# Optimization experiments

Measured on AMD Instinct MI355X. Metric: run time of the kernel, lower is better.

Reference implementation:

```python
import jax, jax.numpy as jnp
import numpy as np

WINDOW_SIZE = 7
L = 255.0
C1 = (0.01 * L) ** 2
C2 = (0.03 * L) ** 2


def _box_filter(x, window):
    # x: [B,1,H,W], window: [1,1,k,k] (uniform 1/k^2). VALID conv, groups=1.
    return jax.lax.conv_general_dilated(
        x, window, window_strides=(1, 1), padding='VALID',
        dimension_numbers=('NCHW', 'OIHW', 'NCHW'))


def setup_inputs() -> dict:
    key = jax.random.key(0)
    k1, k2 = jax.random.split(key)
    shape = (16, 1, 1080, 1920)
    img1 = jax.random.uniform(k1, shape, dtype=jnp.float32) * L
    img2 = jax.random.uniform(k2, shape, dtype=jnp.float32) * L
    window = jnp.ones((1, 1, WINDOW_SIZE, WINDOW_SIZE), dtype=jnp.float32) / (WINDOW_SIZE * WINDOW_SIZE)
    return {"img1": img1, "img2": img2, "window": window}


def reference(img1, img2, window):
    mu1 = _box_filter(img1, window)
    mu2 = _box_filter(img2, window)
    mu1_sq = mu1 * mu1
    mu2_sq = mu2 * mu2
    mu1_mu2 = mu1 * mu2
    sigma1_sq = _box_filter(img1 * img1, window) - mu1_sq
    sigma2_sq = _box_filter(img2 * img2, window) - mu2_sq
    sigma12 = _box_filter(img1 * img2, window) - mu1_mu2
    v1 = 2.0 * sigma12 + C2
    v2 = sigma1_sq + sigma2_sq + C2
    ssim_map = (2.0 * mu1_mu2 + C1) * v1 / ((mu1_sq + mu2_sq + C1) * v2)
    return jnp.mean(ssim_map)
```

## Files before the change

kernel.cpp:

```cpp
#include <hip/hip_runtime.h>


constexpr int W_IN = 1920, H_IN = 1080;
constexpr int WOUT = W_IN - 6;
constexpr int HOUT = H_IN - 6;
constexpr int NBATCH = 16;
constexpr int WCOLS = 244;
constexpr int TW = 4 * WCOLS;
constexpr int TH = 71;
constexpr int NBX = 2, NBY = 16;
constexpr int NBLK = NBX * NBY * NBATCH;

constexpr float C1f = 6.5025f;
constexpr float C2f = 58.5225f;
constexpr float INV49 = 1.0f / 49.0f;

__device__ __forceinline__ float bperm(int addr, float v) {
  return __int_as_float(__builtin_amdgcn_ds_bpermute(addr, __float_as_int(v)));
}

__global__ __attribute__((amdgpu_flat_work_group_size(256, 256),
                          amdgpu_waves_per_eu(2, 2)))
void ssim_kernel(const float* __restrict__ img1, const float* __restrict__ img2,
                 double* __restrict__ partial) {
  const int t = threadIdx.x;
  const int lane = t & 63;
  const int xw = blockIdx.x * TW + (t >> 6) * WCOLS;
  const int y0 = blockIdx.y * TH;
  const size_t ib = (size_t)blockIdx.z * (size_t)(H_IN * W_IN);
  const float* __restrict__ p1 = img1 + ib;
  const float* __restrict__ p2 = img2 + ib;

  const int gcol = min(xw + 4 * lane, W_IN - 4);
  const int up1 = ((lane + 1) & 63) << 2;
  const int up2 = ((lane + 2) & 63) << 2;
  const bool lv = lane < 61;
  const bool m0 = lv && (xw + 4 * lane + 0 < WOUT);
  const bool m1 = lv && (xw + 4 * lane + 1 < WOUT);
  const bool m2 = lv && (xw + 4 * lane + 2 < WOUT);
  const bool m3 = lv && (xw + 4 * lane + 3 < WOUT);

#define DECLR(Q, C)                                                          \
  float R##Q##_##C##_0 = 0.f, R##Q##_##C##_1 = 0.f, R##Q##_##C##_2 = 0.f,    \
        R##Q##_##C##_3 = 0.f, R##Q##_##C##_4 = 0.f, R##Q##_##C##_5 = 0.f,    \
        R##Q##_##C##_6 = 0.f;
  DECLR(1, 0) DECLR(1, 1) DECLR(1, 2) DECLR(1, 3)
  DECLR(2, 0) DECLR(2, 1) DECLR(2, 2) DECLR(2, 3)
  DECLR(3, 0) DECLR(3, 1) DECLR(3, 2) DECLR(3, 3)
  DECLR(4, 0) DECLR(4, 1) DECLR(4, 2) DECLR(4, 3)
  DECLR(5, 0) DECLR(5, 1) DECLR(5, 2) DECLR(5, 3)
#undef DECLR
#define DECLV(Q) float V##Q##_0 = 0.f, V##Q##_1 = 0.f, V##Q##_2 = 0.f, V##Q##_3 = 0.f;
  DECLV(1) DECLV(2) DECLV(3) DECLV(4) DECLV(5)
#undef DECLV

  float accv = 0.f;

  float4 Aa = *(const float4*)(p1 + (size_t)y0 * W_IN + gcol);
  float4 Ab = *(const float4*)(p2 + (size_t)y0 * W_IN + gcol);
  float4 Ba, Bb;
  int gyn = y0 + 1;
  int oy = y0;

#define QC(Q, C, J)                                                         \
  { V##Q##_##C += s - R##Q##_##C##_##J; R##Q##_##C##_##J = s; }

#define EPI1(VA, VB, VAA, VBB, VAB, MASK)                                   \
  {                                                                         \
    const float mu1 = (VA) * INV49, mu2 = (VB) * INV49;                     \
    const float mu1s = mu1 * mu1, mu2s = mu2 * mu2, mu12 = mu1 * mu2;       \
    const float sg1 = fmaf((VAA), INV49, -mu1s);                            \
    const float sg2 = fmaf((VBB), INV49, -mu2s);                            \
    const float sg12 = fmaf((VAB), INV49, -mu12);                           \
    const float v1 = fmaf(2.f, sg12, C2f);                                  \
    const float v2 = sg1 + sg2 + C2f;                                       \
    const float num = fmaf(2.f, mu12, C1f) * v1;                            \
    const float den = (mu1s + mu2s + C1f) * v2;                             \
    const float ss = num * __builtin_amdgcn_rcpf(den);                      \
    accv += (MASK) ? ss : 0.f;                                              \
  }

#define STEP(J, CAa, CAb, NAa, NAb, DO_EPI)                                 \
  {                                                                         \
    NAa = *(const float4*)(p1 + (size_t)gyn * W_IN + gcol);                 \
    NAb = *(const float4*)(p2 + (size_t)gyn * W_IN + gcol);                 \
    gyn = min(gyn + 1, H_IN - 1);                                           \
    const float a1x = bperm(up1, CAa.x), a1y = bperm(up1, CAa.y);           \
    const float a1z = bperm(up1, CAa.z), a1w = bperm(up1, CAa.w);           \
    const float a2x = bperm(up2, CAa.x), a2y = bperm(up2, CAa.y);           \
    const float b1x = bperm(up1, CAb.x), b1y = bperm(up1, CAb.y);           \
    const float b1z = bperm(up1, CAb.z), b1w = bperm(up1, CAb.w);           \
    const float b2x = bperm(up2, CAb.x), b2y = bperm(up2, CAb.y);           \
    float s;                                                                \
    s = ((CAa.x + CAa.y) + (CAa.z + CAa.w)) + ((a1x + a1y) + a1z);          \
    QC(1, 0, J)                                                             \
    s = s - CAa.x + a1w;  QC(1, 1, J)                                       \
    s = s - CAa.y + a2x;  QC(1, 2, J)                                       \
    s = s - CAa.z + a2y;  QC(1, 3, J)                                       \
    s = ((CAb.x + CAb.y) + (CAb.z + CAb.w)) + ((b1x + b1y) + b1z);          \
    QC(2, 0, J)                                                             \
    s = s - CAb.x + b1w;  QC(2, 1, J)                                       \
    s = s - CAb.y + b2x;  QC(2, 2, J)                                       \
    s = s - CAb.z + b2y;  QC(2, 3, J)                                       \
    s = CAa.x * CAa.x;                                                      \
    s = fmaf(CAa.y, CAa.y, s); s = fmaf(CAa.z, CAa.z, s);                   \
    s = fmaf(CAa.w, CAa.w, s); s = fmaf(a1x, a1x, s);                       \
    s = fmaf(a1y, a1y, s); s = fmaf(a1z, a1z, s);                           \
    QC(3, 0, J)                                                             \
    s = fmaf(-CAa.x, CAa.x, fmaf(a1w, a1w, s));  QC(3, 1, J)                \
    s = fmaf(-CAa.y, CAa.y, fmaf(a2x, a2x, s));  QC(3, 2, J)                \
    s = fmaf(-CAa.z, CAa.z, fmaf(a2y, a2y, s));  QC(3, 3, J)                \
    s = CAb.x * CAb.x;                                                      \
    s = fmaf(CAb.y, CAb.y, s); s = fmaf(CAb.z, CAb.z, s);                   \
    s = fmaf(CAb.w, CAb.w, s); s = fmaf(b1x, b1x, s);                       \
    s = fmaf(b1y, b1y, s); s = fmaf(b1z, b1z, s);                           \
    QC(4, 0, J)                                                             \
    s = fmaf(-CAb.x, CAb.x, fmaf(b1w, b1w, s));  QC(4, 1, J)                \
    s = fmaf(-CAb.y, CAb.y, fmaf(b2x, b2x, s));  QC(4, 2, J)                \
    s = fmaf(-CAb.z, CAb.z, fmaf(b2y, b2y, s));  QC(4, 3, J)                \
    s = CAa.x * CAb.x;                                                      \
    s = fmaf(CAa.y, CAb.y, s); s = fmaf(CAa.z, CAb.z, s);                   \
    s = fmaf(CAa.w, CAb.w, s); s = fmaf(a1x, b1x, s);                       \
    s = fmaf(a1y, b1y, s); s = fmaf(a1z, b1z, s);                           \
    QC(5, 0, J)                                                             \
    s = fmaf(-CAa.x, CAb.x, fmaf(a1w, b1w, s));  QC(5, 1, J)                \
    s = fmaf(-CAa.y, CAb.y, fmaf(a2x, b2x, s));  QC(5, 2, J)                \
    s = fmaf(-CAa.z, CAb.z, fmaf(a2y, b2y, s));  QC(5, 3, J)                \
    if (DO_EPI) {                                                           \
      if (oy < HOUT) {                                                      \
        EPI1(V1_0, V2_0, V3_0, V4_0, V5_0, m0)                              \
        EPI1(V1_1, V2_1, V3_1, V4_1, V5_1, m1)                              \
        EPI1(V1_2, V2_2, V3_2, V4_2, V5_2, m2)                              \
        EPI1(V1_3, V2_3, V3_3, V4_3, V5_3, m3)                              \
      }                                                                     \
      ++oy;                                                                 \
    }                                                                       \
  }

  STEP(0, Aa, Ab, Ba, Bb, false)
  STEP(1, Ba, Bb, Aa, Ab, false)
  STEP(2, Aa, Ab, Ba, Bb, false)
  STEP(3, Ba, Bb, Aa, Ab, false)
  STEP(4, Aa, Ab, Ba, Bb, false)
  STEP(5, Ba, Bb, Aa, Ab, false)
  STEP(6, Aa, Ab, Ba, Bb, true)
  for (int gp = 0; gp < 5; ++gp) {
    STEP(0, Ba, Bb, Aa, Ab, true)
    STEP(1, Aa, Ab, Ba, Bb, true)
    STEP(2, Ba, Bb, Aa, Ab, true)
    STEP(3, Aa, Ab, Ba, Bb, true)
    STEP(4, Ba, Bb, Aa, Ab, true)
    STEP(5, Aa, Ab, Ba, Bb, true)
    STEP(6, Ba, Bb, Aa, Ab, true)
    STEP(0, Aa, Ab, Ba, Bb, true)
    STEP(1, Ba, Bb, Aa, Ab, true)
    STEP(2, Aa, Ab, Ba, Bb, true)
    STEP(3, Ba, Bb, Aa, Ab, true)
    STEP(4, Aa, Ab, Ba, Bb, true)
    STEP(5, Ba, Bb, Aa, Ab, true)
    STEP(6, Aa, Ab, Ba, Bb, true)
  }
#undef STEP
#undef QC
#undef EPI1

  __shared__ float wsum[4];
#pragma unroll
  for (int off = 32; off > 0; off >>= 1) accv += __shfl_down(accv, off);
  if ((t & 63) == 0) wsum[t >> 6] = accv;
  __syncthreads();
  if (t == 0) {
    const int bid = blockIdx.x + NBX * (blockIdx.y + NBY * blockIdx.z);
    partial[bid] = (double)wsum[0] + (double)wsum[1] +
                   (double)wsum[2] + (double)wsum[3];
  }
}

__global__ __launch_bounds__(256)
void finalize_kernel(const double* __restrict__ partial,
                     float* __restrict__ out) {
  const int tid = threadIdx.x;
  double s = 0.0;
  for (int i = tid; i < NBLK; i += 256) s += partial[i];
#pragma unroll
  for (int off = 32; off > 0; off >>= 1) s += __shfl_down(s, off);
  __shared__ double ws[4];
  if ((tid & 63) == 0) ws[tid >> 6] = s;
  __syncthreads();
  if (tid == 0) {
    const double tot = ws[0] + ws[1] + ws[2] + ws[3];
    out[0] = (float)(tot / ((double)NBATCH * (double)HOUT * (double)WOUT));
  }
}

extern "C" void kernel_launch(void* const* d_in, const int* in_sizes, int n_in,
                              void* d_out, int out_size, void* d_ws, size_t ws_size,
                              hipStream_t stream) {
  const float* img1 = (const float*)d_in[0];
  const float* img2 = (const float*)d_in[1];
  double* partial = (double*)d_ws;
  dim3 grid(NBX, NBY, NBATCH);
  hipLaunchKernelGGL(ssim_kernel, grid, dim3(256), 0, stream, img1, img2,
                     partial);
  hipLaunchKernelGGL(finalize_kernel, dim3(1), dim3(256), 0, stream, partial,
                     (float*)d_out);
}
```

Measured before the change: 290.6 us.

## Narrow per-lane strip to two columns and double occupancy

Each lane now handles 2 output columns with float2 loads instead of 4 with float4, and the x-grid doubles to cover the image. Register state (ring buffers and vertical sums) is roughly halved, and the waves-per-EU hint rises from 2 to 4 so more waves can hide memory latency. In exchange each lane needs a third bpermute neighbour, so there are more cross-lane shuffles and more redundant halo loads per output column, and smaller global loads per lane.

```diff
diff --git a/kernel.cpp b/kernel.cpp
--- a/kernel.cpp
+++ b/kernel.cpp
@@ -5,10 +5,10 @@
 constexpr int WOUT = W_IN - 6;
 constexpr int HOUT = H_IN - 6;
 constexpr int NBATCH = 16;
-constexpr int WCOLS = 244;
+constexpr int WCOLS = 122;
 constexpr int TW = 4 * WCOLS;
 constexpr int TH = 71;
-constexpr int NBX = 2, NBY = 16;
+constexpr int NBX = 4, NBY = 16;
 constexpr int NBLK = NBX * NBY * NBATCH;
 
 constexpr float C1f = 6.5025f;
@@ -20,7 +20,7 @@
 }
 
 __global__ __attribute__((amdgpu_flat_work_group_size(256, 256),
-                          amdgpu_waves_per_eu(2, 2)))
+                          amdgpu_waves_per_eu(4)))
 void ssim_kernel(const float* __restrict__ img1, const float* __restrict__ img2,
                  double* __restrict__ partial) {
   const int t = threadIdx.x;
@@ -31,34 +31,33 @@
   const float* __restrict__ p1 = img1 + ib;
   const float* __restrict__ p2 = img2 + ib;
 
-  const int gcol = min(xw + 4 * lane, W_IN - 4);
+  const int gcol = min(xw + 2 * lane, W_IN - 2);
   const int up1 = ((lane + 1) & 63) << 2;
   const int up2 = ((lane + 2) & 63) << 2;
+  const int up3 = ((lane + 3) & 63) << 2;
   const bool lv = lane < 61;
-  const bool m0 = lv && (xw + 4 * lane + 0 < WOUT);
-  const bool m1 = lv && (xw + 4 * lane + 1 < WOUT);
-  const bool m2 = lv && (xw + 4 * lane + 2 < WOUT);
-  const bool m3 = lv && (xw + 4 * lane + 3 < WOUT);
+  const bool m0 = lv && (xw + 2 * lane + 0 < WOUT);
+  const bool m1 = lv && (xw + 2 * lane + 1 < WOUT);
 
 #define DECLR(Q, C)                                                          \
   float R##Q##_##C##_0 = 0.f, R##Q##_##C##_1 = 0.f, R##Q##_##C##_2 = 0.f,    \
         R##Q##_##C##_3 = 0.f, R##Q##_##C##_4 = 0.f, R##Q##_##C##_5 = 0.f,    \
         R##Q##_##C##_6 = 0.f;
-  DECLR(1, 0) DECLR(1, 1) DECLR(1, 2) DECLR(1, 3)
-  DECLR(2, 0) DECLR(2, 1) DECLR(2, 2) DECLR(2, 3)
-  DECLR(3, 0) DECLR(3, 1) DECLR(3, 2) DECLR(3, 3)
-  DECLR(4, 0) DECLR(4, 1) DECLR(4, 2) DECLR(4, 3)
-  DECLR(5, 0) DECLR(5, 1) DECLR(5, 2) DECLR(5, 3)
+  DECLR(1, 0) DECLR(1, 1)
+  DECLR(2, 0) DECLR(2, 1)
+  DECLR(3, 0) DECLR(3, 1)
+  DECLR(4, 0) DECLR(4, 1)
+  DECLR(5, 0) DECLR(5, 1)
 #undef DECLR
-#define DECLV(Q) float V##Q##_0 = 0.f, V##Q##_1 = 0.f, V##Q##_2 = 0.f, V##Q##_3 = 0.f;
+#define DECLV(Q) float V##Q##_0 = 0.f, V##Q##_1 = 0.f;
   DECLV(1) DECLV(2) DECLV(3) DECLV(4) DECLV(5)
 #undef DECLV
 
   float accv = 0.f;
 
-  float4 Aa = *(const float4*)(p1 + (size_t)y0 * W_IN + gcol);
-  float4 Ab = *(const float4*)(p2 + (size_t)y0 * W_IN + gcol);
-  float4 Ba, Bb;
+  float2 Aa = *(const float2*)(p1 + (size_t)y0 * W_IN + gcol);
+  float2 Ab = *(const float2*)(p2 + (size_t)y0 * W_IN + gcol);
+  float2 Ba, Bb;
   int gyn = y0 + 1;
   int oy = y0;
 
@@ -82,56 +81,44 @@
 
 #define STEP(J, CAa, CAb, NAa, NAb, DO_EPI)                                 \
   {                                                                         \
-    NAa = *(const float4*)(p1 + (size_t)gyn * W_IN + gcol);                 \
-    NAb = *(const float4*)(p2 + (size_t)gyn * W_IN + gcol);                 \
+    NAa = *(const float2*)(p1 + (size_t)gyn * W_IN + gcol);                 \
+    NAb = *(const float2*)(p2 + (size_t)gyn * W_IN + gcol);                 \
     gyn = min(gyn + 1, H_IN - 1);                                           \
     const float a1x = bperm(up1, CAa.x), a1y = bperm(up1, CAa.y);           \
-    const float a1z = bperm(up1, CAa.z), a1w = bperm(up1, CAa.w);           \
     const float a2x = bperm(up2, CAa.x), a2y = bperm(up2, CAa.y);           \
+    const float a3x = bperm(up3, CAa.x), a3y = bperm(up3, CAa.y);           \
     const float b1x = bperm(up1, CAb.x), b1y = bperm(up1, CAb.y);           \
-    const float b1z = bperm(up1, CAb.z), b1w = bperm(up1, CAb.w);           \
     const float b2x = bperm(up2, CAb.x), b2y = bperm(up2, CAb.y);           \
+    const float b3x = bperm(up3, CAb.x), b3y = bperm(up3, CAb.y);           \
     float s;                                                                \
-    s = ((CAa.x + CAa.y) + (CAa.z + CAa.w)) + ((a1x + a1y) + a1z);          \
+    s = ((CAa.x + CAa.y) + (a1x + a1y)) + ((a2x + a2y) + a3x);              \
     QC(1, 0, J)                                                             \
-    s = s - CAa.x + a1w;  QC(1, 1, J)                                       \
-    s = s - CAa.y + a2x;  QC(1, 2, J)                                       \
-    s = s - CAa.z + a2y;  QC(1, 3, J)                                       \
-    s = ((CAb.x + CAb.y) + (CAb.z + CAb.w)) + ((b1x + b1y) + b1z);          \
+    s = s - CAa.x + a3y;  QC(1, 1, J)                                       \
+    s = ((CAb.x + CAb.y) + (b1x + b1y)) + ((b2x + b2y) + b3x);              \
     QC(2, 0, J)                                                             \
-    s = s - CAb.x + b1w;  QC(2, 1, J)                                       \
-    s = s - CAb.y + b2x;  QC(2, 2, J)                                       \
-    s = s - CAb.z + b2y;  QC(2, 3, J)                                       \
+    s = s - CAb.x + b3y;  QC(2, 1, J)                                       \
     s = CAa.x * CAa.x;                                                      \
-    s = fmaf(CAa.y, CAa.y, s); s = fmaf(CAa.z, CAa.z, s);                   \
-    s = fmaf(CAa.w, CAa.w, s); s = fmaf(a1x, a1x, s);                       \
-    s = fmaf(a1y, a1y, s); s = fmaf(a1z, a1z, s);                           \
+    s = fmaf(CAa.y, CAa.y, s); s = fmaf(a1x, a1x, s);                       \
+    s = fmaf(a1y, a1y, s); s = fmaf(a2x, a2x, s);                           \
+    s = fmaf(a2y, a2y, s); s = fmaf(a3x, a3x, s);                           \
     QC(3, 0, J)                                                             \
-    s = fmaf(-CAa.x, CAa.x, fmaf(a1w, a1w, s));  QC(3, 1, J)                \
-    s = fmaf(-CAa.y, CAa.y, fmaf(a2x, a2x, s));  QC(3, 2, J)                \
-    s = fmaf(-CAa.z, CAa.z, fmaf(a2y, a2y, s));  QC(3, 3, J)                \
+    s = fmaf(-CAa.x, CAa.x, fmaf(a3y, a3y, s));  QC(3, 1, J)                \
     s = CAb.x * CAb.x;                                                      \
-    s = fmaf(CAb.y, CAb.y, s); s = fmaf(CAb.z, CAb.z, s);                   \
-    s = fmaf(CAb.w, CAb.w, s); s = fmaf(b1x, b1x, s);                       \
-    s = fmaf(b1y, b1y, s); s = fmaf(b1z, b1z, s);                           \
+    s = fmaf(CAb.y, CAb.y, s); s = fmaf(b1x, b1x, s);                       \
+    s = fmaf(b1y, b1y, s); s = fmaf(b2x, b2x, s);                           \
+    s = fmaf(b2y, b2y, s); s = fmaf(b3x, b3x, s);                           \
     QC(4, 0, J)                                                             \
-    s = fmaf(-CAb.x, CAb.x, fmaf(b1w, b1w, s));  QC(4, 1, J)                \
-    s = fmaf(-CAb.y, CAb.y, fmaf(b2x, b2x, s));  QC(4, 2, J)                \
-    s = fmaf(-CAb.z, CAb.z, fmaf(b2y, b2y, s));  QC(4, 3, J)                \
+    s = fmaf(-CAb.x, CAb.x, fmaf(b3y, b3y, s));  QC(4, 1, J)                \
     s = CAa.x * CAb.x;                                                      \
-    s = fmaf(CAa.y, CAb.y, s); s = fmaf(CAa.z, CAb.z, s);                   \
-    s = fmaf(CAa.w, CAb.w, s); s = fmaf(a1x, b1x, s);                       \
-    s = fmaf(a1y, b1y, s); s = fmaf(a1z, b1z, s);                           \
+    s = fmaf(CAa.y, CAb.y, s); s = fmaf(a1x, b1x, s);                       \
+    s = fmaf(a1y, b1y, s); s = fmaf(a2x, b2x, s);                           \
+    s = fmaf(a2y, b2y, s); s = fmaf(a3x, b3x, s);                           \
     QC(5, 0, J)                                                             \
-    s = fmaf(-CAa.x, CAb.x, fmaf(a1w, b1w, s));  QC(5, 1, J)                \
-    s = fmaf(-CAa.y, CAb.y, fmaf(a2x, b2x, s));  QC(5, 2, J)                \
-    s = fmaf(-CAa.z, CAb.z, fmaf(a2y, b2y, s));  QC(5, 3, J)                \
+    s = fmaf(-CAa.x, CAb.x, fmaf(a3y, b3y, s));  QC(5, 1, J)                \
     if (DO_EPI) {                                                           \
       if (oy < HOUT) {                                                      \
         EPI1(V1_0, V2_0, V3_0, V4_0, V5_0, m0)                              \
         EPI1(V1_1, V2_1, V3_1, V4_1, V5_1, m1)                              \
-        EPI1(V1_2, V2_2, V3_2, V4_2, V5_2, m2)                              \
-        EPI1(V1_3, V2_3, V3_3, V4_3, V5_3, m3)                              \
       }                                                                     \
       ++oy;                                                                 \
     }                                                                       \
```

After: 294.2 us. No clear change (+1.2%).
